# Kernel tuning notes

Hardware: AMD Instinct MI355X
Metric: run time of the kernel (lower is better)

## Reference

```python
import jax, jax.numpy as jnp
import numpy as np

N = 50000
E = 800000
F_IN = 128
HID = 16
HEADS = 8
C = 16
NEG_SLOPE = 0.2


def setup_inputs() -> dict:
    key = jax.random.key(0)
    ks = jax.random.split(key, 12)
    glorot = lambda k, shape: jax.random.normal(k, shape, jnp.float32) * jnp.sqrt(2.0 / (shape[0] + shape[-1]))
    return {
        "x": jax.random.normal(ks[0], (N, F_IN), jnp.float32),
        "edge_index": jax.random.randint(ks[1], (2, E), 0, N, jnp.int32),
        "x2": jax.random.normal(ks[2], (N, F_IN), jnp.float32),
        "edge_index2": jax.random.randint(ks[3], (2, E), 0, N, jnp.int32),
        # conv1: GATConv(F_IN -> HID, heads=HEADS, concat=True)
        "W1": glorot(ks[4], (F_IN, HEADS * HID)),
        "a1_src": glorot(ks[5], (HEADS, HID)),
        "a1_dst": glorot(ks[6], (HEADS, HID)),
        "b1": jnp.zeros((HEADS * HID,), jnp.float32),
        # conv2: GATConv(HEADS*HID -> C, heads=1, concat=False)
        "W2": glorot(ks[7], (HEADS * HID, 1 * C)),
        "a2_src": glorot(ks[8], (1, C)),
        "a2_dst": glorot(ks[9], (1, C)),
        "b2": jnp.zeros((C,), jnp.float32),
    }


def gat_conv(x, edge_index, W, a_src, a_dst, bias, concat):
    """PyG-style GATConv with self-loops, segment softmax over destinations."""
    n = x.shape[0]
    heads, out = a_src.shape
    h = (x @ W).reshape(n, heads, out)               # [N, H, O]
    loops = jnp.arange(n, dtype=edge_index.dtype)
    src = jnp.concatenate([edge_index[0], loops])     # messages flow src -> dst
    dst = jnp.concatenate([edge_index[1], loops])
    alpha_s = jnp.einsum('nho,ho->nh', h, a_src)
    alpha_d = jnp.einsum('nho,ho->nh', h, a_dst)
    e = jax.nn.leaky_relu(alpha_s[src] + alpha_d[dst], NEG_SLOPE)  # [E+N, H]
    m = jax.lax.stop_gradient(jax.ops.segment_max(e, dst, num_segments=n))
    w = jnp.exp(e - m[dst])
    denom = jax.ops.segment_sum(w, dst, num_segments=n)
    alpha = w / (denom[dst] + 1e-16)                  # segment softmax
    msg = h[src] * alpha[:, :, None]                  # [E+N, H, O]
    agg = jax.ops.segment_sum(msg, dst, num_segments=n)
    agg = agg.reshape(n, heads * out) if concat else agg.mean(axis=1)
    return agg + bias


def forward_once(x, edge_index, W1, a1_src, a1_dst, b1, W2, a2_src, a2_dst, b2):
    # dropout(p=0.6) is identity in eval mode
    h = jax.nn.elu(gat_conv(x, edge_index, W1, a1_src, a1_dst, b1, concat=True))
    return gat_conv(h, edge_index, W2, a2_src, a2_dst, b2, concat=False)


def reference(x, edge_index, x2, edge_index2, W1, a1_src, a1_dst, b1, W2, a2_src, a2_dst, b2):
    y = forward_once(x, edge_index, W1, a1_src, a1_dst, b1, W2, a2_src, a2_dst, b2)
    z = forward_once(x2, edge_index2, W1, a1_src, a1_dst, b1, W2, a2_src, a2_dst, b2)
    eps = 1e-8
    ny = jnp.maximum(jnp.linalg.norm(y, axis=1), eps)
    nz = jnp.maximum(jnp.linalg.norm(z, axis=1), eps)
    cos = jnp.sum(y * z, axis=1) / (ny * nz)
    ls_y = jax.nn.log_softmax(y, axis=1)
    ls_z = jax.nn.log_softmax(z, axis=1)
    return (ls_y, 1.0 - cos, ls_z, ls_y, ls_y)
```

## Files before the change

### kernel.cpp

```cpp
#include <hip/hip_runtime.h>
#include <hip/hip_bf16.h>

#define N_NODES 50000
#define N_EDGES 800000
#define F_INS   128
#define HIDDEN  16
#define HEADS   8
#define HO      128
#define C_OUT   16
#define NEG_SLOPE 0.2f
#define SLOT    64
#define NB_G1   ((N_NODES + 63) / 64)

#define NCLS     128
#define CLS_MUL  1342u
#define CLS_SH   19
#define CAP      8192
#define CHUNK    2048
#define NB_BKT   ((N_EDGES + CHUNK - 1) / CHUNK)

typedef unsigned short u16;
typedef unsigned int   u32;
typedef int v4i __attribute__((ext_vector_type(4)));
typedef short bf16x8 __attribute__((ext_vector_type(8)));
typedef float f32x4 __attribute__((ext_vector_type(4)));

__device__ __forceinline__ float bf2f(u16 u) {
    union { u32 i; float f; } t; t.i = ((u32)u) << 16; return t.f;
}
__device__ __forceinline__ float bflo(u32 q) {
    union { u32 i; float f; } t; t.i = q << 16; return t.f;
}
__device__ __forceinline__ float bfhi(u32 q) {
    union { u32 i; float f; } t; t.i = q & 0xFFFF0000u; return t.f;
}
__device__ __forceinline__ u32 f2bf(float f) {
    union { float f; u32 i; } t; t.f = f;
    u32 x = t.i;
    u32 lsb = (x >> 16) & 1u;
    x += 0x7FFFu + lsb;
    return x >> 16;
}
__device__ __forceinline__ int cls_of(int d) { return (int)(((u32)d * CLS_MUL) >> CLS_SH); }
__host__ __device__ __forceinline__ int cls_base(int c) { return (int)(((u32)c * 524288u + (CLS_MUL - 1)) / CLS_MUL); }

__global__ void k_wt(const float* __restrict__ W1, const float* __restrict__ a1s,
                     const float* __restrict__ a1d, u32* __restrict__ w1t,
                     u32* __restrict__ a1t) {
    int t = threadIdx.x;
    if (blockIdx.x < 32) {
        int e = blockIdx.x * 256 + t;
        int c = e >> 6, kp = e & 63;
        float lo = W1[(2 * kp) * 128 + c];
        float hi = W1[(2 * kp + 1) * 128 + c];
        w1t[e] = (f2bf(hi) << 16) | f2bf(lo);
    } else {
        #pragma unroll
        for (int i = 0; i < 4; ++i) {
            int wi = t + i * 256;
            int n = wi >> 6, kp = wi & 63;
            int h = n >> 1;
            const float* av = ((n & 1) ? a1d : a1s) + h * 16;
            float s0 = 0.f, s1 = 0.f;
            #pragma unroll
            for (int c = 0; c < 16; ++c) {
                s0 += W1[(2 * kp) * 128 + h * 16 + c] * av[c];
                s1 += W1[(2 * kp + 1) * 128 + h * 16 + c] * av[c];
            }
            a1t[wi] = (f2bf(s1) << 16) | f2bf(s0);
        }
    }
}

__launch_bounds__(256)
__global__ void k_bucket(const int* __restrict__ ei0, const int* __restrict__ ei1,
                         int* __restrict__ gcur, u32* __restrict__ bucket) {
    __shared__ int cnt[NCLS];
    __shared__ int base[NCLS];
    int t = threadIdx.x;
    int g = blockIdx.x & 1;
    int chunk = blockIdx.x >> 1;
    int e0 = chunk * CHUNK + t * 8;
    bool act = e0 < N_EDGES;

    if (t < NCLS) cnt[t] = 0;
    __syncthreads();

    const int* src = g ? ei1 : ei0;
    const int* dst = src + N_EDGES;
    int d8[8], s8[8], c8[8];
    if (act) {
        v4i da = *(const v4i*)(dst + e0), db = *(const v4i*)(dst + e0 + 4);
        v4i sa = *(const v4i*)(src + e0), sb = *(const v4i*)(src + e0 + 4);
        d8[0]=da[0]; d8[1]=da[1]; d8[2]=da[2]; d8[3]=da[3];
        d8[4]=db[0]; d8[5]=db[1]; d8[6]=db[2]; d8[7]=db[3];
        s8[0]=sa[0]; s8[1]=sa[1]; s8[2]=sa[2]; s8[3]=sa[3];
        s8[4]=sb[0]; s8[5]=sb[1]; s8[6]=sb[2]; s8[7]=sb[3];
        #pragma unroll
        for (int j = 0; j < 8; ++j) {
            c8[j] = cls_of(d8[j]);
            atomicAdd(&cnt[c8[j]], 1);
        }
    }
    __syncthreads();
    if (t < NCLS) {
        int n = cnt[t];
        base[t] = n ? atomicAdd(&gcur[g * NCLS + t], n) : 0;
        cnt[t] = 0;
    }
    __syncthreads();
    if (act) {
        #pragma unroll
        for (int j = 0; j < 8; ++j) {
            int c = c8[j];
            int p = atomicAdd(&cnt[c], 1);
            bucket[(size_t)(g * NCLS + c) * CAP + base[c] + p] =
                ((u32)d8[j] << 16) | (u32)s8[j];
        }
    }
}

__launch_bounds__(256)
__global__ void k_build(const int* __restrict__ gcur, const u32* __restrict__ bucket,
                        int* __restrict__ cursor, u16* __restrict__ col) {
    __shared__ int cnt[391];
    int t = threadIdx.x;
    int c = blockIdx.x & (NCLS - 1);
    int g = blockIdx.x >> 7;
    int d0 = cls_base(c);
    int d1 = (c == NCLS - 1) ? N_NODES : cls_base(c + 1);
    int nn = d1 - d0;
    for (int j = t; j < nn; j += 256) cnt[j] = 0;
    __syncthreads();

    int size = gcur[g * NCLS + c];
    const u32* bp = bucket + (size_t)(g * NCLS + c) * CAP;
    u16* cl = col + (size_t)g * N_NODES * SLOT;
    for (int i = t; i < size; i += 256) {
        u32 e = bp[i];
        int d = (int)(e >> 16);
        int s = (int)(e & 0xFFFFu);
        int p = atomicAdd(&cnt[d - d0], 1);
        if (p < SLOT) cl[(size_t)d * SLOT + p] = (u16)s;
    }
    __syncthreads();
    int* cur = cursor + g * N_NODES;
    for (int j = t; j < nn; j += 256) cur[d0 + j] = cnt[j];
}

__launch_bounds__(256)
__global__ void k_gemm1(const float* __restrict__ x, const u32* __restrict__ w1t,
                        const u32* __restrict__ a1t, u32* __restrict__ h1b,
                        float* __restrict__ as_, float* __restrict__ ad_) {
    __shared__ u32 xls[4096];
    int t = threadIdx.x;
    int r0 = blockIdx.x * 64;

    const float2* x2p = (const float2*)x;
    #pragma unroll
    for (int i = 0; i < 16; ++i) {
        int A = t + i * 256;
        int wi = A >> 10, kt = (A >> 8) & 3, L = (A >> 2) & 63, jj = A & 3;
        int m = L & 15, qd = L >> 4;
        int r = r0 + wi * 16 + m;
        int pp = kt * 16 + qd * 4 + jj;
        float2 v = make_float2(0.f, 0.f);
        if (r < N_NODES) v = x2p[(size_t)r * 64 + pp];
        xls[A] = (f2bf(v.y) << 16) | f2bf(v.x);
    }
    __syncthreads();

    int lane = t & 63;
    int wid = t >> 6;
    int n = lane & 15, quad = lane >> 4;

    f32x4 acc[8], acca;
    #pragma unroll
    for (int ct = 0; ct < 8; ++ct) acc[ct] = (f32x4){0.f, 0.f, 0.f, 0.f};
    acca = (f32x4){0.f, 0.f, 0.f, 0.f};

    #pragma unroll
    for (int kt = 0; kt < 4; ++kt) {
        union { uint4 u; bf16x8 v; } af;
        af.u = *(const uint4*)(xls + wid * 1024 + kt * 256 + lane * 4);
        #pragma unroll
        for (int ct = 0; ct < 8; ++ct) {
            union { uint4 u; bf16x8 v; } bf_;
            bf_.u = *(const uint4*)(w1t + (ct * 16 + n) * 64 + kt * 16 + quad * 4);
            acc[ct] = __builtin_amdgcn_mfma_f32_16x16x32_bf16(af.v, bf_.v, acc[ct], 0, 0, 0);
        }
        union { uint4 u; bf16x8 v; } ba;
        ba.u = *(const uint4*)(a1t + n * 64 + kt * 16 + quad * 4);
        acca = __builtin_amdgcn_mfma_f32_16x16x32_bf16(af.v, ba.v, acca, 0, 0, 0);
    }

    int h = n >> 1;
    #pragma unroll
    for (int reg = 0; reg < 4; ++reg) {
        int gr = r0 + wid * 16 + quad * 4 + reg;
        bool ok = gr < N_NODES;
        float av = acca[reg];
        if (ok) {
            if (n & 1) ad_[gr * 8 + h] = av;
            else       as_[gr * 8 + h] = av;
        }
        #pragma unroll
        for (int ct = 0; ct < 8; ++ct) {
            u32 my = f2bf(acc[ct][reg]);
            u32 ot = (u32)__shfl_xor((int)my, 1);
            if (!(n & 1) && ok)
                h1b[(size_t)gr * 64 + ct * 8 + (n >> 1)] = (ot << 16) | my;
        }
    }
}

__launch_bounds__(256)
__global__ void k_gat1(const u32* __restrict__ h1b, const float* __restrict__ as_,
                       const float* __restrict__ ad_, const int* __restrict__ cursor,
                       const u16* __restrict__ col, const float* __restrict__ b1,
                       u32* __restrict__ hL1) {
    int lane = threadIdx.x & 63;
    int node = blockIdx.x * 4 + (threadIdx.x >> 6);
    if (node >= N_NODES) return;
    int h = lane >> 3;
    float ad = ad_[node * 8 + h];

    float as0 = as_[node * 8 + h];
    float tt = as0 + ad;
    tt = (tt > 0.f) ? tt : NEG_SLOPE * tt;
    float w = __expf(tt);
    float denom = w;
    u32 q = h1b[(size_t)node * 64 + lane];
    float ax = w * bflo(q), ay = w * bfhi(q);

    int deg = min(cursor[node], SLOT);
    const u16* cp = col + (size_t)node * SLOT;
    int e = 0;
    for (; e + 7 < deg; e += 8) {
        ushort4 sa4 = *(const ushort4*)(cp + e);
        ushort4 sb4 = *(const ushort4*)(cp + e + 4);
        int s0 = sa4.x, s1 = sa4.y, s2 = sa4.z, s3 = sa4.w;
        int s4 = sb4.x, s5 = sb4.y, s6 = sb4.z, s7 = sb4.w;
        float A0 = as_[s0 * 8 + h], A1 = as_[s1 * 8 + h];
        float A2 = as_[s2 * 8 + h], A3 = as_[s3 * 8 + h];
        float A4 = as_[s4 * 8 + h], A5 = as_[s5 * 8 + h];
        float A6 = as_[s6 * 8 + h], A7 = as_[s7 * 8 + h];
        u32 q0 = h1b[(size_t)s0 * 64 + lane], q1 = h1b[(size_t)s1 * 64 + lane];
        u32 q2 = h1b[(size_t)s2 * 64 + lane], q3 = h1b[(size_t)s3 * 64 + lane];
        u32 q4 = h1b[(size_t)s4 * 64 + lane], q5 = h1b[(size_t)s5 * 64 + lane];
        u32 q6 = h1b[(size_t)s6 * 64 + lane], q7 = h1b[(size_t)s7 * 64 + lane];
        float t0 = A0 + ad; t0 = (t0 > 0.f) ? t0 : NEG_SLOPE * t0;
        float t1 = A1 + ad; t1 = (t1 > 0.f) ? t1 : NEG_SLOPE * t1;
        float t2 = A2 + ad; t2 = (t2 > 0.f) ? t2 : NEG_SLOPE * t2;
        float t3 = A3 + ad; t3 = (t3 > 0.f) ? t3 : NEG_SLOPE * t3;
        float t4 = A4 + ad; t4 = (t4 > 0.f) ? t4 : NEG_SLOPE * t4;
        float t5 = A5 + ad; t5 = (t5 > 0.f) ? t5 : NEG_SLOPE * t5;
        float t6 = A6 + ad; t6 = (t6 > 0.f) ? t6 : NEG_SLOPE * t6;
        float t7 = A7 + ad; t7 = (t7 > 0.f) ? t7 : NEG_SLOPE * t7;
        float w0 = __expf(t0), w1 = __expf(t1), w2 = __expf(t2), w3 = __expf(t3);
        float w4 = __expf(t4), w5 = __expf(t5), w6 = __expf(t6), w7 = __expf(t7);
        denom += ((w0 + w1) + (w2 + w3)) + ((w4 + w5) + (w6 + w7));
        ax += w0 * bflo(q0) + w1 * bflo(q1) + w2 * bflo(q2) + w3 * bflo(q3)
            + w4 * bflo(q4) + w5 * bflo(q5) + w6 * bflo(q6) + w7 * bflo(q7);
        ay += w0 * bfhi(q0) + w1 * bfhi(q1) + w2 * bfhi(q2) + w3 * bfhi(q3)
            + w4 * bfhi(q4) + w5 * bfhi(q5) + w6 * bfhi(q6) + w7 * bfhi(q7);
    }
    for (; e + 3 < deg; e += 4) {
        ushort4 s4v = *(const ushort4*)(cp + e);
        int s0 = s4v.x, s1 = s4v.y, s2 = s4v.z, s3 = s4v.w;
        float A0 = as_[s0 * 8 + h], A1 = as_[s1 * 8 + h];
        float A2 = as_[s2 * 8 + h], A3 = as_[s3 * 8 + h];
        u32 q0 = h1b[(size_t)s0 * 64 + lane], q1 = h1b[(size_t)s1 * 64 + lane];
        u32 q2 = h1b[(size_t)s2 * 64 + lane], q3 = h1b[(size_t)s3 * 64 + lane];
        float t0 = A0 + ad; t0 = (t0 > 0.f) ? t0 : NEG_SLOPE * t0;
        float t1 = A1 + ad; t1 = (t1 > 0.f) ? t1 : NEG_SLOPE * t1;
        float t2 = A2 + ad; t2 = (t2 > 0.f) ? t2 : NEG_SLOPE * t2;
        float t3 = A3 + ad; t3 = (t3 > 0.f) ? t3 : NEG_SLOPE * t3;
        float w0 = __expf(t0), w1 = __expf(t1), w2 = __expf(t2), w3 = __expf(t3);
        denom += (w0 + w1) + (w2 + w3);
        ax += w0 * bflo(q0) + w1 * bflo(q1) + w2 * bflo(q2) + w3 * bflo(q3);
        ay += w0 * bfhi(q0) + w1 * bfhi(q1) + w2 * bfhi(q2) + w3 * bfhi(q3);
    }
    for (; e < deg; ++e) {
        int s = cp[e];
        float A = as_[s * 8 + h];
        u32 qq = h1b[(size_t)s * 64 + lane];
        float t0 = A + ad; t0 = (t0 > 0.f) ? t0 : NEG_SLOPE * t0;
        float w0 = __expf(t0);
        denom += w0;
        ax += w0 * bflo(qq);
        ay += w0 * bfhi(qq);
    }
    float inv = 1.f / (denom + 1e-16f);
    int c = lane * 2;
    float o0 = ax * inv + b1[c];
    float o1 = ay * inv + b1[c + 1];
    o0 = (o0 > 0.f) ? o0 : (__expf(o0) - 1.f);
    o1 = (o1 > 0.f) ? o1 : (__expf(o1) - 1.f);
    hL1[(size_t)node * 64 + lane] = (f2bf(o1) << 16) | f2bf(o0);
}

__launch_bounds__(256)
__global__ void k_gemm2(const u16* __restrict__ hL1, const float* __restrict__ W2,
                        const float* __restrict__ a2s, const float* __restrict__ a2d,
                        float* __restrict__ h2, float* __restrict__ as2,
                        float* __restrict__ ad2) {
    __shared__ float w2s[F_INS * C_OUT];
    __shared__ float hs[16 * 136];
    int t = threadIdx.x;

    const float4* w4 = (const float4*)W2;
    #pragma unroll
    for (int i = 0; i < 2; ++i) {
        int idx = t + i * 256;
        ((float4*)w2s)[idx] = w4[idx];
    }
    int r0 = blockIdx.x * 16;
    const ushort4* hg = (const ushort4*)hL1;
    #pragma unroll
    for (int i = 0; i < 2; ++i) {
        int idx = t + i * 256;
        int r  = idx >> 5;
        int c4 = idx & 31;
        ushort4 q = make_ushort4(0, 0, 0, 0);
        if (r0 + r < N_NODES) q = hg[(size_t)(r0 + r) * 32 + c4];
        float4 v; v.x = bf2f(q.x); v.y = bf2f(q.y); v.z = bf2f(q.z); v.w = bf2f(q.w);
        *(float4*)(hs + r * 136 + c4 * 4) = v;
    }
    __syncthreads();

    int c = t & 15, r = t >> 4;
    float acc = 0.f;
    #pragma unroll 8
    for (int k = 0; k < F_INS; ++k) acc += hs[r * 136 + k] * w2s[k * C_OUT + c];
    int n = r0 + r;
    if (n < N_NODES) h2[(size_t)n * C_OUT + c] = acc;

    float sa = acc * a2s[c];
    float sd = acc * a2d[c];
    #pragma unroll
    for (int m = 1; m < 16; m <<= 1) {
        sa += __shfl_xor(sa, m);
        sd += __shfl_xor(sd, m);
    }
    if (c == 0 && n < N_NODES) { as2[n] = sa; ad2[n] = sd; }
}

__device__ __forceinline__ void gat2_accum(const float* __restrict__ h2,
                                           const float* __restrict__ as2, float ad,
                                           const u16* __restrict__ cp, int deg, int c,
                                           float& denom, float& acc) {
    int e = 0;
    for (; e + 7 < deg; e += 8) {
        ushort4 sa4 = *(const ushort4*)(cp + e);
        ushort4 sb4 = *(const ushort4*)(cp + e + 4);
        int s0 = sa4.x, s1 = sa4.y, s2 = sa4.z, s3 = sa4.w;
        int s4 = sb4.x, s5 = sb4.y, s6 = sb4.z, s7 = sb4.w;
        float A0 = as2[s0], A1 = as2[s1], A2 = as2[s2], A3 = as2[s3];
        float A4 = as2[s4], A5 = as2[s5], A6 = as2[s6], A7 = as2[s7];
        float v0 = h2[(size_t)s0 * C_OUT + c], v1 = h2[(size_t)s1 * C_OUT + c];
        float v2 = h2[(size_t)s2 * C_OUT + c], v3 = h2[(size_t)s3 * C_OUT + c];
        float v4 = h2[(size_t)s4 * C_OUT + c], v5 = h2[(size_t)s5 * C_OUT + c];
        float v6 = h2[(size_t)s6 * C_OUT + c], v7 = h2[(size_t)s7 * C_OUT + c];
        float t0 = A0 + ad; t0 = (t0 > 0.f) ? t0 : NEG_SLOPE * t0;
        float t1 = A1 + ad; t1 = (t1 > 0.f) ? t1 : NEG_SLOPE * t1;
        float t2 = A2 + ad; t2 = (t2 > 0.f) ? t2 : NEG_SLOPE * t2;
        float t3 = A3 + ad; t3 = (t3 > 0.f) ? t3 : NEG_SLOPE * t3;
        float t4 = A4 + ad; t4 = (t4 > 0.f) ? t4 : NEG_SLOPE * t4;
        float t5 = A5 + ad; t5 = (t5 > 0.f) ? t5 : NEG_SLOPE * t5;
        float t6 = A6 + ad; t6 = (t6 > 0.f) ? t6 : NEG_SLOPE * t6;
        float t7 = A7 + ad; t7 = (t7 > 0.f) ? t7 : NEG_SLOPE * t7;
        float w0 = __expf(t0), w1 = __expf(t1), w2 = __expf(t2), w3 = __expf(t3);
        float w4 = __expf(t4), w5 = __expf(t5), w6 = __expf(t6), w7 = __expf(t7);
        denom += ((w0 + w1) + (w2 + w3)) + ((w4 + w5) + (w6 + w7));
        acc += (w0 * v0 + w1 * v1 + w2 * v2 + w3 * v3)
             + (w4 * v4 + w5 * v5 + w6 * v6 + w7 * v7);
    }
    for (; e + 3 < deg; e += 4) {
        ushort4 s4v = *(const ushort4*)(cp + e);
        int s0 = s4v.x, s1 = s4v.y, s2 = s4v.z, s3 = s4v.w;
        float A0 = as2[s0], A1 = as2[s1], A2 = as2[s2], A3 = as2[s3];
        float v0 = h2[(size_t)s0 * C_OUT + c], v1 = h2[(size_t)s1 * C_OUT + c];
        float v2 = h2[(size_t)s2 * C_OUT + c], v3 = h2[(size_t)s3 * C_OUT + c];
        float t0 = A0 + ad; t0 = (t0 > 0.f) ? t0 : NEG_SLOPE * t0;
        float t1 = A1 + ad; t1 = (t1 > 0.f) ? t1 : NEG_SLOPE * t1;
        float t2 = A2 + ad; t2 = (t2 > 0.f) ? t2 : NEG_SLOPE * t2;
        float t3 = A3 + ad; t3 = (t3 > 0.f) ? t3 : NEG_SLOPE * t3;
        float w0 = __expf(t0), w1 = __expf(t1), w2 = __expf(t2), w3 = __expf(t3);
        denom += (w0 + w1) + (w2 + w3);
        acc += w0 * v0 + w1 * v1 + w2 * v2 + w3 * v3;
    }
    for (; e < deg; ++e) {
        int s = cp[e];
        float t0 = as2[s] + ad; t0 = (t0 > 0.f) ? t0 : NEG_SLOPE * t0;
        float w0 = __expf(t0);
        denom += w0;
        acc += w0 * h2[(size_t)s * C_OUT + c];
    }
}

__launch_bounds__(256)
__global__ void k_gat2(const float* __restrict__ h2, const float* __restrict__ as2,
                       const float* __restrict__ ad2, const int* __restrict__ cursor,
                       const u16* __restrict__ col, const float* __restrict__ b2,
                       float* __restrict__ yout) {
    int t = threadIdx.x;
    int node = blockIdx.x * 16 + (t >> 4);
    int c = t & 15;
    if (node >= N_NODES) return;
    float ad = ad2[node];

    float tt = as2[node] + ad;
    tt = (tt > 0.f) ? tt : NEG_SLOPE * tt;
    float w = __expf(tt);
    float denom = w;
    float acc = w * h2[(size_t)node * C_OUT + c];

    int deg = min(cursor[node], SLOT);
    gat2_accum(h2, as2, ad, col + (size_t)node * SLOT, deg, c, denom, acc);
    yout[(size_t)node * C_OUT + c] = acc / (denom + 1e-16f) + b2[c];
}

__launch_bounds__(256)
__global__ void k_gat2f(const float* __restrict__ h2, const float* __restrict__ as2,
                        const float* __restrict__ ad2, const int* __restrict__ cursor,
                        const u16* __restrict__ col, const float* __restrict__ b2,
                        const float* __restrict__ yb, float* __restrict__ out) {
    int t = threadIdx.x;
    int node = blockIdx.x * 16 + (t >> 4);
    int c = t & 15;
    if (node >= N_NODES) return;
    float ad = ad2[node];

    float tt = as2[node] + ad;
    tt = (tt > 0.f) ? tt : NEG_SLOPE * tt;
    float w = __expf(tt);
    float denom = w;
    float acc = w * h2[(size_t)node * C_OUT + c];

    int deg = min(cursor[node], SLOT);
    gat2_accum(h2, as2, ad, col + (size_t)node * SLOT, deg, c, denom, acc);
    float zv = acc / (denom + 1e-16f) + b2[c];
    float yv = yb[(size_t)node * C_OUT + c];

    float my = yv, mz = zv;
    #pragma unroll
    for (int m = 1; m < 16; m <<= 1) {
        my = fmaxf(my, __shfl_xor(my, m));
        mz = fmaxf(mz, __shfl_xor(mz, m));
    }
    float sy = __expf(yv - my), sz = __expf(zv - mz);
    float dot = yv * zv, ny = yv * yv, nz = zv * zv;
    #pragma unroll
    for (int m = 1; m < 16; m <<= 1) {
        sy  += __shfl_xor(sy, m);
        sz  += __shfl_xor(sz, m);
        dot += __shfl_xor(dot, m);
        ny  += __shfl_xor(ny, m);
        nz  += __shfl_xor(nz, m);
    }
    float lsey = my + __logf(sy);
    float lsez = mz + __logf(sz);
    float omc = 1.f - dot / (fmaxf(sqrtf(ny), 1e-8f) * fmaxf(sqrtf(nz), 1e-8f));

    const int O1 = N_NODES * C_OUT;
    const int O2 = O1 + N_NODES;
    const int O3 = O2 + N_NODES * C_OUT;
    const int O4 = O3 + N_NODES * C_OUT;
    float ly = yv - lsey;
    float lz = zv - lsez;
    int base = node * 16 + c;
    out[base]      = ly;
    out[O2 + base] = lz;
    out[O3 + base] = ly;
    out[O4 + base] = ly;
    if (c == 0) out[O1 + node] = omc;
}

extern "C" void kernel_launch(void* const* d_in, const int* in_sizes, int n_in,
                              void* d_out, int out_size, void* d_ws, size_t ws_size,
                              hipStream_t stream) {
    (void)in_sizes; (void)n_in; (void)out_size; (void)ws_size;
    const float* x1  = (const float*)d_in[0];
    const int*   ei1 = (const int*)d_in[1];
    const float* x2  = (const float*)d_in[2];
    const int*   ei2 = (const int*)d_in[3];
    const float* W1  = (const float*)d_in[4];
    const float* a1s = (const float*)d_in[5];
    const float* a1d = (const float*)d_in[6];
    const float* b1  = (const float*)d_in[7];
    const float* W2  = (const float*)d_in[8];
    const float* a2s = (const float*)d_in[9];
    const float* a2d = (const float*)d_in[10];
    const float* b2  = (const float*)d_in[11];
    float* out = (float*)d_out;

    char* p = (char*)d_ws;
    int* gcur      = (int*)p; p += (size_t)2 * NCLS * 4;
    u32* w1t       = (u32*)p; p += (size_t)128 * 64 * 4;
    u32* a1t       = (u32*)p; p += (size_t)16 * 64 * 4;
    int* cursor    = (int*)p; p += (size_t)2 * N_NODES * 4;
    u16* col       = (u16*)p; p += (size_t)2 * N_NODES * SLOT * 2;
    float* as1  = (float*)p; p += (size_t)N_NODES * HEADS * 4;
    float* ad1  = (float*)p; p += (size_t)N_NODES * HEADS * 4;
    float* h2   = (float*)p; p += (size_t)N_NODES * C_OUT * 4;
    float* as2  = (float*)p; p += (size_t)N_NODES * 4;
    float* ad2  = (float*)p; p += (size_t)N_NODES * 4;
    float* yb   = (float*)p; p += (size_t)N_NODES * C_OUT * 4;
    u32* hL1    = (u32*)p;   p += (size_t)N_NODES * HO * 2;
    u32* h1b    = (u32*)p;   p += (size_t)N_NODES * HO * 2;
    u32* bucket = h1b;

    hipMemsetAsync(gcur, 0, (size_t)2 * NCLS * 4, stream);
    k_wt    <<<33, 256, 0, stream>>>(W1, a1s, a1d, w1t, a1t);
    k_bucket<<<2 * NB_BKT, 256, 0, stream>>>(ei1, ei2, gcur, bucket);
    k_build <<<2 * NCLS, 256, 0, stream>>>(gcur, bucket, cursor, col);

    for (int g = 0; g < 2; ++g) {
        const float* x = g ? x2 : x1;
        int* cur_g = cursor + g * N_NODES;
        u16* col_g = col + (size_t)g * N_NODES * SLOT;
        k_gemm1<<<NB_G1, 256, 0, stream>>>(x, w1t, a1t, h1b, as1, ad1);
        k_gat1 <<<(N_NODES + 3) / 4, 256, 0, stream>>>(h1b, as1, ad1, cur_g, col_g, b1, hL1);
        k_gemm2<<<(N_NODES + 15) / 16, 256, 0, stream>>>((const u16*)hL1, W2, a2s, a2d, h2, as2, ad2);
        if (g == 0) {
            k_gat2 <<<(N_NODES + 15) / 16, 256, 0, stream>>>(h2, as2, ad2, cur_g, col_g, b2, yb);
        } else {
            k_gat2f<<<(N_NODES + 15) / 16, 256, 0, stream>>>(h2, as2, ad2, cur_g, col_g, b2, yb, out);
        }
    }
}
```

Measured before the change: 339.9 us.

## Batch both graph passes into single launches and pad neighbor lists with sentinel node

The two forward passes now run as single kernel launches with doubled grids, and per-graph buffers are laid out side by side. The two final GAT2 passes are merged into one kernel that computes y and z together. Neighbor lists are padded to multiples of 8 with a dummy node whose attention score is -1e30, so the gather loops have no tail handling. In k_gat1 each lane computes one edge weight and spreads it with ds_bpermute instead of every lane recomputing all eight exps. The cost is extra padded gathers of the dummy row and some extra workspace.

```diff
diff --git a/kernel.cpp b/kernel.cpp
--- a/kernel.cpp
+++ b/kernel.cpp
@@ -11,6 +11,15 @@
 #define NEG_SLOPE 0.2f
 #define SLOT    64
 #define NB_G1   ((N_NODES + 63) / 64)
+#define NB_GAT1 ((N_NODES + 3) / 4)
+#define NB_G2   ((N_NODES + 16) / 16)
+
+#define NP      50016
+#define AS_ST   ((size_t)NP * 8)
+#define H1B_ST  ((size_t)NP * 64)
+#define HL1_ST  ((size_t)N_NODES * 64)
+#define H2_ST   ((size_t)NP * 16)
+#define AS2_ST  ((size_t)NP)
 
 #define NCLS     128
 #define CLS_MUL  1342u
@@ -40,6 +49,9 @@
     u32 lsb = (x >> 16) & 1u;
     x += 0x7FFFu + lsb;
     return x >> 16;
+}
+__device__ __forceinline__ float lrelu(float t) {
+    return fmaxf(t, NEG_SLOPE * t);
 }
 __device__ __forceinline__ int cls_of(int d) { return (int)(((u32)d * CLS_MUL) >> CLS_SH); }
 __host__ __device__ __forceinline__ int cls_base(int c) { return (int)(((u32)c * 524288u + (CLS_MUL - 1)) / CLS_MUL); }
@@ -145,16 +157,32 @@
     }
     __syncthreads();
     int* cur = cursor + g * N_NODES;
-    for (int j = t; j < nn; j += 256) cur[d0 + j] = cnt[j];
+    for (int j = t; j < nn; j += 256) {
+        int d = d0 + j;
+        int raw = cnt[j];
+        int n0 = min(raw, SLOT);
+        int n1 = (n0 + 7) & ~7;
+        u16* cw = cl + (size_t)d * SLOT;
+        for (int p = n0; p < n1; ++p) cw[p] = (u16)N_NODES;
+        cur[d] = raw;
+    }
 }
 
 __launch_bounds__(256)
-__global__ void k_gemm1(const float* __restrict__ x, const u32* __restrict__ w1t,
-                        const u32* __restrict__ a1t, u32* __restrict__ h1b,
-                        float* __restrict__ as_, float* __restrict__ ad_) {
+__global__ void k_gemm1(const float* __restrict__ x1g, const float* __restrict__ x2g,
+                        const u32* __restrict__ w1t, const u32* __restrict__ a1t,
+                        u32* __restrict__ h1b, float* __restrict__ as_,
+                        float* __restrict__ ad_) {
     __shared__ u32 xls[4096];
     int t = threadIdx.x;
-    int r0 = blockIdx.x * 64;
+    int bid = blockIdx.x;
+    int g = bid >= NB_G1;
+    if (g) bid -= NB_G1;
+    const float* x = g ? x2g : x1g;
+    u32*   h1o = h1b + (size_t)g * H1B_ST;
+    float* aso = as_ + (size_t)g * AS_ST;
+    float* ado = ad_ + (size_t)g * AS_ST;
+    int r0 = bid * 64;
 
     const float2* x2p = (const float2*)x;
     #pragma unroll
@@ -198,18 +226,18 @@
     #pragma unroll
     for (int reg = 0; reg < 4; ++reg) {
         int gr = r0 + wid * 16 + quad * 4 + reg;
-        bool ok = gr < N_NODES;
-        float av = acca[reg];
+        bool ok = gr <= N_NODES;
+        float av = (gr == N_NODES) ? -1e30f : acca[reg];
         if (ok) {
-            if (n & 1) ad_[gr * 8 + h] = av;
-            else       as_[gr * 8 + h] = av;
+            if (n & 1) ado[gr * 8 + h] = av;
+            else       aso[gr * 8 + h] = av;
         }
         #pragma unroll
         for (int ct = 0; ct < 8; ++ct) {
             u32 my = f2bf(acc[ct][reg]);
             u32 ot = (u32)__shfl_xor((int)my, 1);
             if (!(n & 1) && ok)
-                h1b[(size_t)gr * 64 + ct * 8 + (n >> 1)] = (ot << 16) | my;
+                h1o[(size_t)gr * 64 + ct * 8 + (n >> 1)] = (ot << 16) | my;
         }
     }
 }
@@ -219,77 +247,64 @@
                        const float* __restrict__ ad_, const int* __restrict__ cursor,
                        const u16* __restrict__ col, const float* __restrict__ b1,
                        u32* __restrict__ hL1) {
-    int lane = threadIdx.x & 63;
-    int node = blockIdx.x * 4 + (threadIdx.x >> 6);
-    if (node >= N_NODES) return;
-    int h = lane >> 3;
-    float ad = ad_[node * 8 + h];
-
-    float as0 = as_[node * 8 + h];
-    float tt = as0 + ad;
-    tt = (tt > 0.f) ? tt : NEG_SLOPE * tt;
-    float w = __expf(tt);
+    int t = threadIdx.x;
+    int lane = t & 63;
+    int bid = blockIdx.x;
+    int g = bid >= NB_GAT1;
+    if (g) bid -= NB_GAT1;
+    int node = bid * 4 + (t >> 6);
+
+    const u32*   h1  = h1b + (size_t)g * H1B_ST;
+    const float* as1 = as_ + (size_t)g * AS_ST;
+    const float* ad1 = ad_ + (size_t)g * AS_ST;
+    const u16*   cp  = col + ((size_t)g * N_NODES + node) * SLOT;
+
+    int hc = lane >> 3;
+    int ha = lane & 7;
+    int j8 = lane >> 3;
+    int vb = hc << 2;
+
+    float ad_a = ad1[node * 8 + ha];
+    float as_c = as1[node * 8 + hc];
+    float ad_c = ad1[node * 8 + hc];
+
+    float w = __expf(lrelu(as_c + ad_c));
     float denom = w;
-    u32 q = h1b[(size_t)node * 64 + lane];
+    u32 q = h1[(u32)node * 64 + (u32)lane];
     float ax = w * bflo(q), ay = w * bfhi(q);
 
-    int deg = min(cursor[node], SLOT);
-    const u16* cp = col + (size_t)node * SLOT;
-    int e = 0;
-    for (; e + 7 < deg; e += 8) {
+    int deg = min(cursor[g * N_NODES + node], SLOT);
+    int nb = (deg + 7) >> 3;
+    for (int b = 0; b < nb; ++b) {
+        int e = b * 8;
         ushort4 sa4 = *(const ushort4*)(cp + e);
         ushort4 sb4 = *(const ushort4*)(cp + e + 4);
-        int s0 = sa4.x, s1 = sa4.y, s2 = sa4.z, s3 = sa4.w;
-        int s4 = sb4.x, s5 = sb4.y, s6 = sb4.z, s7 = sb4.w;
-        float A0 = as_[s0 * 8 + h], A1 = as_[s1 * 8 + h];
-        float A2 = as_[s2 * 8 + h], A3 = as_[s3 * 8 + h];
-        float A4 = as_[s4 * 8 + h], A5 = as_[s5 * 8 + h];
-        float A6 = as_[s6 * 8 + h], A7 = as_[s7 * 8 + h];
-        u32 q0 = h1b[(size_t)s0 * 64 + lane], q1 = h1b[(size_t)s1 * 64 + lane];
-        u32 q2 = h1b[(size_t)s2 * 64 + lane], q3 = h1b[(size_t)s3 * 64 + lane];
-        u32 q4 = h1b[(size_t)s4 * 64 + lane], q5 = h1b[(size_t)s5 * 64 + lane];
-        u32 q6 = h1b[(size_t)s6 * 64 + lane], q7 = h1b[(size_t)s7 * 64 + lane];
-        float t0 = A0 + ad; t0 = (t0 > 0.f) ? t0 : NEG_SLOPE * t0;
-        float t1 = A1 + ad; t1 = (t1 > 0.f) ? t1 : NEG_SLOPE * t1;
-        float t2 = A2 + ad; t2 = (t2 > 0.f) ? t2 : NEG_SLOPE * t2;
-        float t3 = A3 + ad; t3 = (t3 > 0.f) ? t3 : NEG_SLOPE * t3;
-        float t4 = A4 + ad; t4 = (t4 > 0.f) ? t4 : NEG_SLOPE * t4;
-        float t5 = A5 + ad; t5 = (t5 > 0.f) ? t5 : NEG_SLOPE * t5;
-        float t6 = A6 + ad; t6 = (t6 > 0.f) ? t6 : NEG_SLOPE * t6;
-        float t7 = A7 + ad; t7 = (t7 > 0.f) ? t7 : NEG_SLOPE * t7;
-        float w0 = __expf(t0), w1 = __expf(t1), w2 = __expf(t2), w3 = __expf(t3);
-        float w4 = __expf(t4), w5 = __expf(t5), w6 = __expf(t6), w7 = __expf(t7);
+        u32 q0 = h1[((u32)sa4.x << 6) | (u32)lane];
+        u32 q1 = h1[((u32)sa4.y << 6) | (u32)lane];
+        u32 q2 = h1[((u32)sa4.z << 6) | (u32)lane];
+        u32 q3 = h1[((u32)sa4.w << 6) | (u32)lane];
+        u32 q4 = h1[((u32)sb4.x << 6) | (u32)lane];
+        u32 q5 = h1[((u32)sb4.y << 6) | (u32)lane];
+        u32 q6 = h1[((u32)sb4.z << 6) | (u32)lane];
+        u32 q7 = h1[((u32)sb4.w << 6) | (u32)lane];
+
+        int sA = cp[e + j8];
+        float A = as1[sA * 8 + ha];
+        int wli = __float_as_int(__expf(lrelu(A + ad_a)));
+        float w0 = __int_as_float(__builtin_amdgcn_ds_bpermute(vb,       wli));
+        float w1 = __int_as_float(__builtin_amdgcn_ds_bpermute(vb + 32,  wli));
+        float w2 = __int_as_float(__builtin_amdgcn_ds_bpermute(vb + 64,  wli));
+        float w3 = __int_as_float(__builtin_amdgcn_ds_bpermute(vb + 96,  wli));
+        float w4 = __int_as_float(__builtin_amdgcn_ds_bpermute(vb + 128, wli));
+        float w5 = __int_as_float(__builtin_amdgcn_ds_bpermute(vb + 160, wli));
+        float w6 = __int_as_float(__builtin_amdgcn_ds_bpermute(vb + 192, wli));
+        float w7 = __int_as_float(__builtin_amdgcn_ds_bpermute(vb + 224, wli));
+
         denom += ((w0 + w1) + (w2 + w3)) + ((w4 + w5) + (w6 + w7));
         ax += w0 * bflo(q0) + w1 * bflo(q1) + w2 * bflo(q2) + w3 * bflo(q3)
             + w4 * bflo(q4) + w5 * bflo(q5) + w6 * bflo(q6) + w7 * bflo(q7);
         ay += w0 * bfhi(q0) + w1 * bfhi(q1) + w2 * bfhi(q2) + w3 * bfhi(q3)
             + w4 * bfhi(q4) + w5 * bfhi(q5) + w6 * bfhi(q6) + w7 * bfhi(q7);
-    }
-    for (; e + 3 < deg; e += 4) {
-        ushort4 s4v = *(const ushort4*)(cp + e);
-        int s0 = s4v.x, s1 = s4v.y, s2 = s4v.z, s3 = s4v.w;
-        float A0 = as_[s0 * 8 + h], A1 = as_[s1 * 8 + h];
-        float A2 = as_[s2 * 8 + h], A3 = as_[s3 * 8 + h];
-        u32 q0 = h1b[(size_t)s0 * 64 + lane], q1 = h1b[(size_t)s1 * 64 + lane];
-        u32 q2 = h1b[(size_t)s2 * 64 + lane], q3 = h1b[(size_t)s3 * 64 + lane];
-        float t0 = A0 + ad; t0 = (t0 > 0.f) ? t0 : NEG_SLOPE * t0;
-        float t1 = A1 + ad; t1 = (t1 > 0.f) ? t1 : NEG_SLOPE * t1;
-        float t2 = A2 + ad; t2 = (t2 > 0.f) ? t2 : NEG_SLOPE * t2;
-        float t3 = A3 + ad; t3 = (t3 > 0.f) ? t3 : NEG_SLOPE * t3;
-        float w0 = __expf(t0), w1 = __expf(t1), w2 = __expf(t2), w3 = __expf(t3);
-        denom += (w0 + w1) + (w2 + w3);
-        ax += w0 * bflo(q0) + w1 * bflo(q1) + w2 * bflo(q2) + w3 * bflo(q3);
-        ay += w0 * bfhi(q0) + w1 * bfhi(q1) + w2 * bfhi(q2) + w3 * bfhi(q3);
-    }
-    for (; e < deg; ++e) {
-        int s = cp[e];
-        float A = as_[s * 8 + h];
-        u32 qq = h1b[(size_t)s * 64 + lane];
-        float t0 = A + ad; t0 = (t0 > 0.f) ? t0 : NEG_SLOPE * t0;
-        float w0 = __expf(t0);
-        denom += w0;
-        ax += w0 * bflo(qq);
-        ay += w0 * bfhi(qq);
     }
     float inv = 1.f / (denom + 1e-16f);
     int c = lane * 2;
@@ -297,17 +312,24 @@
     float o1 = ay * inv + b1[c + 1];
     o0 = (o0 > 0.f) ? o0 : (__expf(o0) - 1.f);
     o1 = (o1 > 0.f) ? o1 : (__expf(o1) - 1.f);
-    hL1[(size_t)node * 64 + lane] = (f2bf(o1) << 16) | f2bf(o0);
+    hL1[(size_t)g * HL1_ST + (size_t)node * 64 + lane] = (f2bf(o1) << 16) | f2bf(o0);
 }
 
 __launch_bounds__(256)
-__global__ void k_gemm2(const u16* __restrict__ hL1, const float* __restrict__ W2,
+__global__ void k_gemm2(const u32* __restrict__ hL1, const float* __restrict__ W2,
                         const float* __restrict__ a2s, const float* __restrict__ a2d,
                         float* __restrict__ h2, float* __restrict__ as2,
                         float* __restrict__ ad2) {
     __shared__ float w2s[F_INS * C_OUT];
     __shared__ float hs[16 * 136];
     int t = threadIdx.x;
+    int bid = blockIdx.x;
+    int g = bid >= NB_G2;
+    if (g) bid -= NB_G2;
+    const u16* hL = (const u16*)(hL1 + (size_t)g * HL1_ST);
+    float* h2o  = h2  + (size_t)g * H2_ST;
+    float* as2o = as2 + (size_t)g * AS2_ST;
+    float* ad2o = ad2 + (size_t)g * AS2_ST;
 
     const float4* w4 = (const float4*)W2;
     #pragma unroll
@@ -315,16 +337,16 @@
         int idx = t + i * 256;
         ((float4*)w2s)[idx] = w4[idx];
     }
-    int r0 = blockIdx.x * 16;
-    const ushort4* hg = (const ushort4*)hL1;
+    int r0 = bid * 16;
+    const ushort4* hg = (const ushort4*)hL;
     #pragma unroll
     for (int i = 0; i < 2; ++i) {
         int idx = t + i * 256;
         int r  = idx >> 5;
         int c4 = idx & 31;
-        ushort4 q = make_ushort4(0, 0, 0, 0);
-        if (r0 + r < N_NODES) q = hg[(size_t)(r0 + r) * 32 + c4];
-        float4 v; v.x = bf2f(q.x); v.y = bf2f(q.y); v.z = bf2f(q.z); v.w = bf2f(q.w);
+        ushort4 qq = make_ushort4(0, 0, 0, 0);
+        if (r0 + r < N_NODES) qq = hg[(size_t)(r0 + r) * 32 + c4];
+        float4 v; v.x = bf2f(qq.x); v.y = bf2f(qq.y); v.z = bf2f(qq.z); v.w = bf2f(qq.w);
         *(float4*)(hs + r * 136 + c4 * 4) = v;
     }
     __syncthreads();
@@ -334,7 +356,7 @@
     #pragma unroll 8
     for (int k = 0; k < F_INS; ++k) acc += hs[r * 136 + k] * w2s[k * C_OUT + c];
     int n = r0 + r;
-    if (n < N_NODES) h2[(size_t)n * C_OUT + c] = acc;
+    if (n <= N_NODES) h2o[(size_t)n * C_OUT + c] = acc;
 
     float sa = acc * a2s[c];
     float sd = acc * a2d[c];
@@ -343,105 +365,62 @@
         sa += __shfl_xor(sa, m);
         sd += __shfl_xor(sd, m);
     }
-    if (c == 0 && n < N_NODES) { as2[n] = sa; ad2[n] = sd; }
-}
-
-__device__ __forceinline__ void gat2_accum(const float* __restrict__ h2,
-                                           const float* __restrict__ as2, float ad,
-                                           const u16* __restrict__ cp, int deg, int c,
-                                           float& denom, float& acc) {
-    int e = 0;
-    for (; e + 7 < deg; e += 8) {
-        ushort4 sa4 = *(const ushort4*)(cp + e);
-        ushort4 sb4 = *(const ushort4*)(cp + e + 4);
+    if (c == 0 && n <= N_NODES) {
+        as2o[n] = (n == N_NODES) ? -1e30f : sa;
+        ad2o[n] = sd;
+    }
+}
+
+__device__ __forceinline__ float gat2_node(const float* __restrict__ h2g,
+                                           const float* __restrict__ as2g,
+                                           const float* __restrict__ ad2g,
+                                           const int* __restrict__ curg,
+                                           const u16* __restrict__ cp,
+                                           const float* __restrict__ b2,
+                                           int node, int c) {
+    float ad = ad2g[node];
+    float w = __expf(lrelu(as2g[node] + ad));
+    float denom = w;
+    float acc = w * h2g[(u32)node * C_OUT + (u32)c];
+
+    int deg = min(curg[node], SLOT);
+    int nb = (deg + 7) >> 3;
+    for (int b = 0; b < nb; ++b) {
+        const u16* ce = cp + b * 8;
+        ushort4 sa4 = *(const ushort4*)ce;
+        ushort4 sb4 = *(const ushort4*)(ce + 4);
         int s0 = sa4.x, s1 = sa4.y, s2 = sa4.z, s3 = sa4.w;
         int s4 = sb4.x, s5 = sb4.y, s6 = sb4.z, s7 = sb4.w;
-        float A0 = as2[s0], A1 = as2[s1], A2 = as2[s2], A3 = as2[s3];
-        float A4 = as2[s4], A5 = as2[s5], A6 = as2[s6], A7 = as2[s7];
-        float v0 = h2[(size_t)s0 * C_OUT + c], v1 = h2[(size_t)s1 * C_OUT + c];
-        float v2 = h2[(size_t)s2 * C_OUT + c], v3 = h2[(size_t)s3 * C_OUT + c];
-        float v4 = h2[(size_t)s4 * C_OUT + c], v5 = h2[(size_t)s5 * C_OUT + c];
-        float v6 = h2[(size_t)s6 * C_OUT + c], v7 = h2[(size_t)s7 * C_OUT + c];
-        float t0 = A0 + ad; t0 = (t0 > 0.f) ? t0 : NEG_SLOPE * t0;
-        float t1 = A1 + ad; t1 = (t1 > 0.f) ? t1 : NEG_SLOPE * t1;
-        float t2 = A2 + ad; t2 = (t2 > 0.f) ? t2 : NEG_SLOPE * t2;
-        float t3 = A3 + ad; t3 = (t3 > 0.f) ? t3 : NEG_SLOPE * t3;
-        float t4 = A4 + ad; t4 = (t4 > 0.f) ? t4 : NEG_SLOPE * t4;
-        float t5 = A5 + ad; t5 = (t5 > 0.f) ? t5 : NEG_SLOPE * t5;
-        float t6 = A6 + ad; t6 = (t6 > 0.f) ? t6 : NEG_SLOPE * t6;
-        float t7 = A7 + ad; t7 = (t7 > 0.f) ? t7 : NEG_SLOPE * t7;
-        float w0 = __expf(t0), w1 = __expf(t1), w2 = __expf(t2), w3 = __expf(t3);
-        float w4 = __expf(t4), w5 = __expf(t5), w6 = __expf(t6), w7 = __expf(t7);
+        float A0 = as2g[s0], A1 = as2g[s1], A2 = as2g[s2], A3 = as2g[s3];
+        float A4 = as2g[s4], A5 = as2g[s5], A6 = as2g[s6], A7 = as2g[s7];
+        float v0 = h2g[(u32)(s0 * C_OUT + c)], v1 = h2g[(u32)(s1 * C_OUT + c)];
+        float v2 = h2g[(u32)(s2 * C_OUT + c)], v3 = h2g[(u32)(s3 * C_OUT + c)];
+        float v4 = h2g[(u32)(s4 * C_OUT + c)], v5 = h2g[(u32)(s5 * C_OUT + c)];
+        float v6 = h2g[(u32)(s6 * C_OUT + c)], v7 = h2g[(u32)(s7 * C_OUT + c)];
+        float w0 = __expf(lrelu(A0 + ad)), w1 = __expf(lrelu(A1 + ad));
+        float w2 = __expf(lrelu(A2 + ad)), w3 = __expf(lrelu(A3 + ad));
+        float w4 = __expf(lrelu(A4 + ad)), w5 = __expf(lrelu(A5 + ad));
+        float w6 = __expf(lrelu(A6 + ad)), w7 = __expf(lrelu(A7 + ad));
         denom += ((w0 + w1) + (w2 + w3)) + ((w4 + w5) + (w6 + w7));
         acc += (w0 * v0 + w1 * v1 + w2 * v2 + w3 * v3)
              + (w4 * v4 + w5 * v5 + w6 * v6 + w7 * v7);
     }
-    for (; e + 3 < deg; e += 4) {
-        ushort4 s4v = *(const ushort4*)(cp + e);
-        int s0 = s4v.x, s1 = s4v.y, s2 = s4v.z, s3 = s4v.w;
-        float A0 = as2[s0], A1 = as2[s1], A2 = as2[s2], A3 = as2[s3];
-        float v0 = h2[(size_t)s0 * C_OUT + c], v1 = h2[(size_t)s1 * C_OUT + c];
-        float v2 = h2[(size_t)s2 * C_OUT + c], v3 = h2[(size_t)s3 * C_OUT + c];
-        float t0 = A0 + ad; t0 = (t0 > 0.f) ? t0 : NEG_SLOPE * t0;
-        float t1 = A1 + ad; t1 = (t1 > 0.f) ? t1 : NEG_SLOPE * t1;
-        float t2 = A2 + ad; t2 = (t2 > 0.f) ? t2 : NEG_SLOPE * t2;
-        float t3 = A3 + ad; t3 = (t3 > 0.f) ? t3 : NEG_SLOPE * t3;
-        float w0 = __expf(t0), w1 = __expf(t1), w2 = __expf(t2), w3 = __expf(t3);
-        denom += (w0 + w1) + (w2 + w3);
-        acc += w0 * v0 + w1 * v1 + w2 * v2 + w3 * v3;
-    }
-    for (; e < deg; ++e) {
-        int s = cp[e];
-        float t0 = as2[s] + ad; t0 = (t0 > 0.f) ? t0 : NEG_SLOPE * t0;
-        float w0 = __expf(t0);
-        denom += w0;
-        acc += w0 * h2[(size_t)s * C_OUT + c];
-    }
+    return acc / (denom + 1e-16f) + b2[c];
 }
 
 __launch_bounds__(256)
-__global__ void k_gat2(const float* __restrict__ h2, const float* __restrict__ as2,
-                       const float* __restrict__ ad2, const int* __restrict__ cursor,
-                       const u16* __restrict__ col, const float* __restrict__ b2,
-                       float* __restrict__ yout) {
+__global__ void k_gat2e(const float* __restrict__ h2, const float* __restrict__ as2,
+                        const float* __restrict__ ad2, const int* __restrict__ cursor,
+                        const u16* __restrict__ col, const float* __restrict__ b2,
+                        float* __restrict__ out) {
     int t = threadIdx.x;
     int node = blockIdx.x * 16 + (t >> 4);
     int c = t & 15;
-    if (node >= N_NODES) return;
-    float ad = ad2[node];
-
-    float tt = as2[node] + ad;
-    tt = (tt > 0.f) ? tt : NEG_SLOPE * tt;
-    float w = __expf(tt);
-    float denom = w;
-    float acc = w * h2[(size_t)node * C_OUT + c];
-
-    int deg = min(cursor[node], SLOT);
-    gat2_accum(h2, as2, ad, col + (size_t)node * SLOT, deg, c, denom, acc);
-    yout[(size_t)node * C_OUT + c] = acc / (denom + 1e-16f) + b2[c];
-}
-
-__launch_bounds__(256)
-__global__ void k_gat2f(const float* __restrict__ h2, const float* __restrict__ as2,
-                        const float* __restrict__ ad2, const int* __restrict__ cursor,
-                        const u16* __restrict__ col, const float* __restrict__ b2,
-                        const float* __restrict__ yb, float* __restrict__ out) {
-    int t = threadIdx.x;
-    int node = blockIdx.x * 16 + (t >> 4);
-    int c = t & 15;
-    if (node >= N_NODES) return;
-    float ad = ad2[node];
-
-    float tt = as2[node] + ad;
-    tt = (tt > 0.f) ? tt : NEG_SLOPE * tt;
-    float w = __expf(tt);
-    float denom = w;
-    float acc = w * h2[(size_t)node * C_OUT + c];
-
-    int deg = min(cursor[node], SLOT);
-    gat2_accum(h2, as2, ad, col + (size_t)node * SLOT, deg, c, denom, acc);
-    float zv = acc / (denom + 1e-16f) + b2[c];
-    float yv = yb[(size_t)node * C_OUT + c];
+
+    float yv = gat2_node(h2, as2, ad2, cursor,
+                         col + (size_t)node * SLOT, b2, node, c);
+    float zv = gat2_node(h2 + H2_ST, as2 + AS2_ST, ad2 + AS2_ST, cursor + N_NODES,
+                         col + ((size_t)N_NODES + node) * SLOT, b2, node, c);
 
     float my = yv, mz = zv;
     #pragma unroll
@@ -501,32 +480,21 @@
     u32* a1t       = (u32*)p; p += (size_t)16 * 64 * 4;
     int* cursor    = (int*)p; p += (size_t)2 * N_NODES * 4;
     u16* col       = (u16*)p; p += (size_t)2 * N_NODES * SLOT * 2;
-    float* as1  = (float*)p; p += (size_t)N_NODES * HEADS * 4;
-    float* ad1  = (float*)p; p += (size_t)N_NODES * HEADS * 4;
-    float* h2   = (float*)p; p += (size_t)N_NODES * C_OUT * 4;
-    float* as2  = (float*)p; p += (size_t)N_NODES * 4;
-    float* ad2  = (float*)p; p += (size_t)N_NODES * 4;
-    float* yb   = (float*)p; p += (size_t)N_NODES * C_OUT * 4;
-    u32* hL1    = (u32*)p;   p += (size_t)N_NODES * HO * 2;
-    u32* h1b    = (u32*)p;   p += (size_t)N_NODES * HO * 2;
+    float* as1  = (float*)p; p += (size_t)2 * AS_ST * 4;
+    float* ad1  = (float*)p; p += (size_t)2 * AS_ST * 4;
+    float* h2   = (float*)p; p += (size_t)2 * H2_ST * 4;
+    float* as2  = (float*)p; p += (size_t)2 * AS2_ST * 4;
+    float* ad2  = (float*)p; p += (size_t)2 * AS2_ST * 4;
+    u32* hL1    = (u32*)p;   p += (size_t)2 * HL1_ST * 4;
+    u32* h1b    = (u32*)p;   p += (size_t)2 * H1B_ST * 4;
     u32* bucket = h1b;
 
     hipMemsetAsync(gcur, 0, (size_t)2 * NCLS * 4, stream);
     k_wt    <<<33, 256, 0, stream>>>(W1, a1s, a1d, w1t, a1t);
     k_bucket<<<2 * NB_BKT, 256, 0, stream>>>(ei1, ei2, gcur, bucket);
     k_build <<<2 * NCLS, 256, 0, stream>>>(gcur, bucket, cursor, col);
-
-    for (int g = 0; g < 2; ++g) {
-        const float* x = g ? x2 : x1;
-        int* cur_g = cursor + g * N_NODES;
-        u16* col_g = col + (size_t)g * N_NODES * SLOT;
-        k_gemm1<<<NB_G1, 256, 0, stream>>>(x, w1t, a1t, h1b, as1, ad1);
-        k_gat1 <<<(N_NODES + 3) / 4, 256, 0, stream>>>(h1b, as1, ad1, cur_g, col_g, b1, hL1);
-        k_gemm2<<<(N_NODES + 15) / 16, 256, 0, stream>>>((const u16*)hL1, W2, a2s, a2d, h2, as2, ad2);
-        if (g == 0) {
-            k_gat2 <<<(N_NODES + 15) / 16, 256, 0, stream>>>(h2, as2, ad2, cur_g, col_g, b2, yb);
-        } else {
-            k_gat2f<<<(N_NODES + 15) / 16, 256, 0, stream>>>(h2, as2, ad2, cur_g, col_g, b2, yb, out);
-        }
-    }
-}
+    k_gemm1 <<<2 * NB_G1, 256, 0, stream>>>(x1, x2, w1t, a1t, h1b, as1, ad1);
+    k_gat1  <<<2 * NB_GAT1, 256, 0, stream>>>(h1b, as1, ad1, cursor, col, b1, hL1);
+    k_gemm2 <<<2 * NB_G2, 256, 0, stream>>>(hL1, W2, a2s, a2d, h2, as2, ad2);
+    k_gat2e <<<N_NODES / 16, 256, 0, stream>>>(h2, as2, ad2, cursor, col, b2, out);
+}
```

Result: faster. 318.4 us (-6.3%).
